# Optimization experiments

Hardware: AMD Instinct MI355X
Metric: run time of the kernel (lower is better)

Reference implementation:

```python
import jax, jax.numpy as jnp
import numpy as np

BN_EPS = 1e-5
GRID_W = 17  # conv output width hardcoded via lat_idx*17+lon_idx

def _conv(x, w, b, stride):
    y = jax.lax.conv_general_dilated(x, w, (stride, stride), [(1, 1), (1, 1)],
                                     dimension_numbers=("NCHW", "OIHW", "NCHW"))
    return y + b[None, :, None, None]

def _bn_eval(x, g, b):
    # running_mean=0, running_var=1 (fresh BatchNorm in eval mode)
    inv = jnp.float32(1.0 / np.sqrt(1.0 + BN_EPS))
    return x * (g[None, :, None, None] * inv) + b[None, :, None, None]

def setup_inputs() -> dict:
    key = jax.random.key(0)
    ks = iter(jax.random.split(key, 64))
    def rn(shape, s=0.05):
        return jax.random.normal(next(ks), shape, jnp.float32) * s
    B, S, K = 512, 128, 64
    NR = 100000
    inp = {}
    inp["roads"] = jax.random.randint(next(ks), (B, S), 0, NR)
    inp["ratios"] = jax.random.uniform(next(ks), (B, S), jnp.float32) * 0.9 + 0.1
    inp["T"] = jax.random.normal(next(ks), (1, 1, 138, 138), jnp.float32)
    inp["lon_idx"] = jax.random.randint(next(ks), (B, K), 0, 17)
    inp["lat_idx"] = jax.random.randint(next(ks), (B, K), 0, 17)
    inp["lengths"] = jax.random.uniform(next(ks), (NR,), jnp.float32) * 100.0 + 1.0
    inp["map_u"] = jnp.arange(NR, dtype=jnp.int32)
    inp["map_s1"] = jax.random.randint(next(ks), (NR,), 0, 14)
    inp["map_s2"] = jax.random.randint(next(ks), (NR,), 0, 7)
    inp["map_s3"] = jax.random.randint(next(ks), (NR,), 0, 2)
    inp["emb_u"] = rn((NR, 128))
    inp["emb_s1"] = rn((14, 16)); inp["emb_s2"] = rn((7, 8)); inp["emb_s3"] = rn((2, 4))
    inp["rho_w1"] = rn((156, 512)); inp["rho_b1"] = jnp.zeros((512,), jnp.float32)
    inp["rho_w21"] = rn((512, 128)); inp["rho_b21"] = jnp.zeros((128,), jnp.float32)
    inp["conv1_w"] = rn((32, 1, 5, 5)); inp["conv1_b"] = jnp.zeros((32,), jnp.float32)
    inp["bn1_g"] = jnp.ones((32,), jnp.float32); inp["bn1_b"] = jnp.zeros((32,), jnp.float32)
    inp["conv2_w"] = rn((64, 32, 4, 4)); inp["conv2_b"] = jnp.zeros((64,), jnp.float32)
    inp["bn2_g"] = jnp.ones((64,), jnp.float32); inp["bn2_b"] = jnp.zeros((64,), jnp.float32)
    inp["conv3_w"] = rn((128, 64, 4, 4)); inp["conv3_b"] = jnp.zeros((128,), jnp.float32)
    inp["bn3_g"] = jnp.ones((128,), jnp.float32); inp["bn3_b"] = jnp.zeros((128,), jnp.float32)
    inp["f2_w1"] = rn((128, 256)); inp["f2_b1"] = jnp.zeros((256,), jnp.float32)
    inp["f2_w2"] = rn((256, 128)); inp["f2_b2"] = jnp.zeros((128,), jnp.float32)
    inp["f_w1"] = rn((256, 512)); inp["f_b1"] = jnp.zeros((512,), jnp.float32)
    inp["f_w21"] = rn((512, 1)); inp["f_b21"] = jnp.zeros((1,), jnp.float32)
    inp["f_w22"] = rn((512, 1)); inp["f_b22"] = jnp.zeros((1,), jnp.float32)
    return inp

def reference(roads, ratios, T, lon_idx, lat_idx, lengths, map_u, map_s1, map_s2, map_s3,
              emb_u, emb_s1, emb_s2, emb_s3, rho_w1, rho_b1, rho_w21, rho_b21,
              conv1_w, conv1_b, bn1_g, bn1_b, conv2_w, conv2_b, bn2_g, bn2_b,
              conv3_w, conv3_b, bn3_g, bn3_b, f2_w1, f2_b1, f2_w2, f2_b2,
              f_w1, f_b1, f_w21, f_b21, f_w22, f_b22):
    # road lengths / weights
    road_lens = lengths[roads] * ratios               # (B,S)
    l = road_lens.sum(axis=1)                         # (B,)
    w = road_lens / l[:, None]                        # (B,S)
    # ProbRho (eval: dropout=id, reparameterize -> mu)
    u = emb_u[map_u[roads]]                           # (B,S,128)
    s1 = emb_s1[map_s1[roads]]; s2 = emb_s2[map_s2[roads]]; s3 = emb_s3[map_s3[roads]]
    x = jnp.concatenate([u, s1, s2, s3], axis=2)      # (B,S,156)
    h = jax.nn.relu(x @ rho_w1 + rho_b1)
    rho = h @ rho_w21 + rho_b21                       # (B,S,128)
    # ProbTraffic_spatial conv stack
    t = jax.nn.leaky_relu(_bn_eval(_conv(T, conv1_w, conv1_b, 2), bn1_g, bn1_b), 0.1)
    t = jax.nn.leaky_relu(_bn_eval(_conv(t, conv2_w, conv2_b, 2), bn2_g, bn2_b), 0.1)
    t = jax.nn.leaky_relu(_bn_eval(_conv(t, conv3_w, conv3_b, 2), bn3_g, bn3_b), 0.1)  # (1,128,17,17)
    c_flat = jnp.transpose(t[0], (1, 2, 0)).reshape(-1, t.shape[1])  # (289,128)
    # fused segment gather + mean over each trajectory's grid cells
    idx = lat_idx * GRID_W + lon_idx                  # (B,K)
    c_mean = c_flat[idx].mean(axis=1)                 # (B,128)
    h2 = jax.nn.selu(c_mean @ f2_w1 + f2_b1)
    c2 = h2 @ f2_w2 + f2_b2                           # (B,128)
    # ProbTravelTime
    xcat = jnp.concatenate([rho, jnp.broadcast_to(c2[:, None, :], rho.shape)], axis=2)  # (B,S,256)
    h3 = jax.nn.relu(xcat @ f_w1 + f_b1)              # (B,S,512)
    logm = (h3 @ f_w21 + f_b21)[..., 0]               # (B,S)
    logv = (h3 @ f_w22 + f_b22)[..., 0]
    logw = jnp.log(w)
    logm_agg = jax.nn.logsumexp(logm + logw, axis=1)
    logv_agg = jax.nn.logsumexp(logv + 2.0 * logw, axis=1)
    logl = jnp.log(l)
    logmu = logl - logm_agg
    loglam = logl - 3.0 * logm_agg - logv_agg
    return (logmu, loglam)
```

## Files before the change

kernel.cpp:

```cpp
#include <hip/hip_runtime.h>
#include <math.h>

#define BB 512
#define SS 128
#define NROWS (BB*SS)
#define TMG 128
#define NBLKG (NROWS/TMG)

__device__ __forceinline__ float leaky01(float x){ return x >= 0.f ? x : 0.1f*x; }

#define BN_INV 0.9999950000374997f
#define SELU_A 1.6732632423543772f
#define SELU_S 1.0507009873554805f

typedef __attribute__((ext_vector_type(8))) short short8;
typedef __attribute__((ext_vector_type(4))) float f32x4;

__device__ __forceinline__ unsigned short f2bf(float f) {
    unsigned int u = __float_as_uint(f);
    u += 0x7fff + ((u >> 16) & 1);
    return (unsigned short)(u >> 16);
}
__device__ __forceinline__ uint2 pack4bf(float a, float b, float c, float d) {
    uint2 r;
    r.x = (unsigned int)f2bf(a) | ((unsigned int)f2bf(b) << 16);
    r.y = (unsigned int)f2bf(c) | ((unsigned int)f2bf(d) << 16);
    return r;
}

__device__ __forceinline__ unsigned short* xsp(unsigned short* base, int row, int col) {
    unsigned off = (unsigned)(row*384 + col*2);
    off ^= (unsigned)((row & 7) << 4);
    return (unsigned short*)((char*)base + off);
}
__device__ __forceinline__ unsigned short* h1p(unsigned short* base, int row, int col) {
    unsigned off = (unsigned)(row*1024 + col*2);
    off ^= (unsigned)((row & 7) << 4);
    return (unsigned short*)((char*)base + off);
}
__device__ __forceinline__ unsigned short* xcp(unsigned short* base, int row, int col) {
    unsigned off = (unsigned)(row*512 + col*2);
    off ^= (unsigned)((row & 7) << 4);
    return (unsigned short*)((char*)base + off);
}

#define PREP_N (278528 + 32768 + 131072)
#define PREP_BLOCKS (PREP_N/256)
#define CONV1_BLOCKS 578

__global__ __launch_bounds__(256) void combo1_kernel(
    const float* __restrict__ w1, const float* __restrict__ w21, const float* __restrict__ fw1,
    unsigned short* __restrict__ sw1, unsigned short* __restrict__ sw21, unsigned short* __restrict__ sw3,
    const float* __restrict__ c2w_in, const float* __restrict__ c3w_in,
    float* __restrict__ w2t, float* __restrict__ w3t,
    const float* __restrict__ T, const float* __restrict__ cw,
    const float* __restrict__ cbias, const float* __restrict__ g,
    const float* __restrict__ bb, float* __restrict__ out)
{
    if (blockIdx.x < PREP_BLOCKS) {
        int t = blockIdx.x*256 + threadIdx.x;
        if (t < 81920) {
            int j = t & 7; int r = t >> 3; int lane = r & 63; r >>= 6;
            int ks = r % 5; int nt = r / 5;
            int n = nt*16 + (lane & 15);
            int k = ks*32 + (lane >> 4)*8 + j;
            float v = (k < 156) ? w1[k*512 + n] : 0.f;
            sw1[t] = f2bf(v);
        } else if (t < 147456) {
            int u = t - 81920;
            int j = u & 7; int r = u >> 3; int lane = r & 63; r >>= 6;
            int ks = r & 15; int nt = r >> 4;
            int d = nt*16 + (lane & 15);
            int k = ks*32 + (lane >> 4)*8 + j;
            sw21[u] = f2bf(w21[k*128 + d]);
        } else if (t < 278528) {
            int u = t - 147456;
            int j = u & 7; int r = u >> 3; int lane = r & 63; r >>= 6;
            int ks = r & 7; int nt = r >> 3;
            int n = nt*16 + (lane & 15);
            int k = ks*32 + (lane >> 4)*8 + j;
            sw3[u] = f2bf(fw1[k*512 + n]);
        } else if (t < 278528 + 32768) {
            int u = t - 278528;
            int oc = u >> 9; int r = u & 511;
            int kk = r >> 5; int ic = r & 31;
            w2t[u] = c2w_in[oc*512 + ic*16 + kk];
        } else {
            int u = t - (278528 + 32768);
            int oc = u >> 10; int r = u & 1023;
            int kk = r >> 6; int ic = r & 63;
            w3t[u] = c3w_in[oc*1024 + ic*16 + kk];
        }
    } else {
        int t = (blockIdx.x - PREP_BLOCKS)*256 + threadIdx.x;
        if (t >= 32*68*68) return;
        int oc  = t & 31;
        int pos = t >> 5;
        int oy = pos / 68, ox = pos % 68;
        float acc = cbias[oc];
        #pragma unroll
        for (int ky=0; ky<5; ++ky) {
            int iy = oy*2 - 1 + ky;
            if (iy < 0 || iy >= 138) continue;
            #pragma unroll
            for (int kx=0; kx<5; ++kx) {
                int ix = ox*2 - 1 + kx;
                if (ix < 0 || ix >= 138) continue;
                acc += cw[oc*25 + ky*5 + kx] * T[iy*138 + ix];
            }
        }
        acc = acc * (g[oc]*BN_INV) + bb[oc];
        out[pos*32 + oc] = leaky01(acc);
    }
}

__global__ __launch_bounds__(256) void conv2_kernel(
    const float* __restrict__ in,
    const float* __restrict__ w2t,
    const float* __restrict__ bias, const float* __restrict__ g,
    const float* __restrict__ bb, float* __restrict__ out)
{
    int gid = blockIdx.x*256 + threadIdx.x;
    if (gid >= 64*34*34*4) return;
    int icg = gid & 3;
    int o   = gid >> 2;
    int oc  = o & 63;
    int pos = o >> 6;
    int oy = pos / 34, ox = pos % 34;
    float acc = 0.f;
    #pragma unroll
    for (int ky=0; ky<4; ++ky) {
        int iy = oy*2 - 1 + ky;
        if (iy < 0 || iy >= 68) continue;
        #pragma unroll
        for (int kx=0; kx<4; ++kx) {
            int ix = ox*2 - 1 + kx;
            if (ix < 0 || ix >= 68) continue;
            const float* ip = &in[(iy*68+ix)*32 + icg*8];
            const float* wp = &w2t[oc*512 + (ky*4+kx)*32 + icg*8];
            float4 i0 = *(const float4*)ip, i1 = *(const float4*)(ip+4);
            float4 w0 = *(const float4*)wp, w1v = *(const float4*)(wp+4);
            acc += i0.x*w0.x + i0.y*w0.y + i0.z*w0.z + i0.w*w0.w
                 + i1.x*w1v.x + i1.y*w1v.y + i1.z*w1v.z + i1.w*w1v.w;
        }
    }
    acc += __shfl_xor(acc, 1, 64);
    acc += __shfl_xor(acc, 2, 64);
    if (icg == 0) {
        acc = (acc + bias[oc]) * (g[oc]*BN_INV) + bb[oc];
        out[pos*64 + oc] = leaky01(acc);
    }
}

__global__ __launch_bounds__(256) void conv3_kernel(
    const float* __restrict__ in,
    const float* __restrict__ w3t,
    const float* __restrict__ bias, const float* __restrict__ g,
    const float* __restrict__ bb, float* __restrict__ outT)
{
    int gid = blockIdx.x*256 + threadIdx.x;
    if (gid >= 128*289*8) return;
    int icg = gid & 7;
    int o   = gid >> 3;
    int oc  = o & 127;
    int pos = o >> 7;
    int oy = pos / 17, ox = pos % 17;
    float acc = 0.f;
    #pragma unroll
    for (int ky=0; ky<4; ++ky) {
        int iy = oy*2 - 1 + ky;
        if (iy < 0 || iy >= 34) continue;
        #pragma unroll
        for (int kx=0; kx<4; ++kx) {
            int ix = ox*2 - 1 + kx;
            if (ix < 0 || ix >= 34) continue;
            const float* ip = &in[(iy*34+ix)*64 + icg*8];
            const float* wp = &w3t[oc*1024 + (ky*4+kx)*64 + icg*8];
            float4 i0 = *(const float4*)ip, i1 = *(const float4*)(ip+4);
            float4 w0 = *(const float4*)wp, w1v = *(const float4*)(wp+4);
            acc += i0.x*w0.x + i0.y*w0.y + i0.z*w0.z + i0.w*w0.w
                 + i1.x*w1v.x + i1.y*w1v.y + i1.z*w1v.z + i1.w*w1v.w;
        }
    }
    acc += __shfl_xor(acc, 1, 64);
    acc += __shfl_xor(acc, 2, 64);
    acc += __shfl_xor(acc, 4, 64);
    if (icg == 0) {
        acc = (acc + bias[oc]) * (g[oc]*BN_INV) + bb[oc];
        outT[pos*128 + oc] = leaky01(acc);
    }
}

__global__ __launch_bounds__(256) void cmh2c2_kernel(
    const float* __restrict__ t3T, const int* __restrict__ lat, const int* __restrict__ lon,
    const float* __restrict__ w1, const float* __restrict__ b1,
    const float* __restrict__ w2, const float* __restrict__ b2,
    float* __restrict__ c2b)
{
    __shared__ int   ps[64];
    __shared__ float part[256];
    __shared__ float cms[128];
    __shared__ float h2s[256];
    const int b = blockIdx.x;
    const int tid = threadIdx.x;
    if (tid < 64) ps[tid] = lat[b*64+tid]*17 + lon[b*64+tid];
    __syncthreads();
    {
        int d = tid & 127, half = tid >> 7;
        float s = 0.f;
        #pragma unroll 8
        for (int k=0; k<32; ++k) s += t3T[ps[half*32+k]*128 + d];
        part[tid] = s;
    }
    __syncthreads();
    if (tid < 128) cms[tid] = (part[tid] + part[tid+128]) * (1.f/64.f);
    __syncthreads();
    {
        float acc = b1[tid];
        #pragma unroll 8
        for (int k=0; k<128; ++k) acc += cms[k] * w1[k*256 + tid];
        h2s[tid] = acc > 0.f ? SELU_S*acc : SELU_S*SELU_A*(expf(acc)-1.f);
    }
    __syncthreads();
    {
        int d = tid & 127, half = tid >> 7;
        float acc = 0.f;
        #pragma unroll 8
        for (int k=0; k<128; ++k) acc += h2s[half*128 + k] * w2[(half*128+k)*128 + d];
        part[tid] = acc;
    }
    __syncthreads();
    if (tid < 128) c2b[b*128 + tid] = part[tid] + part[tid+128] + b2[tid];
}

__global__ __launch_bounds__(1024, 4) void mega_kernel(
    const int* __restrict__ roads, const float* __restrict__ ratios,
    const float* __restrict__ lengths,
    const int* __restrict__ map_u, const int* __restrict__ map_s1,
    const int* __restrict__ map_s2, const int* __restrict__ map_s3,
    const float* __restrict__ emb_u, const float* __restrict__ emb_s1,
    const float* __restrict__ emb_s2, const float* __restrict__ emb_s3,
    const unsigned short* __restrict__ sw1, const float* __restrict__ b1,
    const unsigned short* __restrict__ sw21, const float* __restrict__ b21,
    const float* __restrict__ c2,
    const unsigned short* __restrict__ sw3, const float* __restrict__ fb1,
    const float* __restrict__ fw21, const float* __restrict__ fb21,
    const float* __restrict__ fw22, const float* __restrict__ fb22,
    float* __restrict__ out)
{
    __shared__ unsigned short buf[65536];
    float* pmv = (float*)buf;
    float* fin = (float*)buf + 4096;

    const int tid  = threadIdx.x;
    const int wid  = tid >> 6;
    const int lane = tid & 63;
    const int lo   = lane & 15;
    const int hi   = lane >> 4;
    const int b    = blockIdx.x;
    const int r0   = b * TMG;

    short8 afp[2];
    #pragma unroll
    for (int mt=0;mt<2;++mt)
        afp[mt] = *(const short8*)&sw1[((wid*2+mt)*5 + 0)*512 + lane*8];

    {
        int row = tid >> 3, seg = tid & 7;
        int road = roads[r0 + row];
        const float* src = emb_u + (long)map_u[road]*128 + seg*16;
        #pragma unroll
        for (int i=0;i<4;++i) {
            float4 v = *(const float4*)&src[i*4];
            *(uint2*)xsp(buf, row, seg*16 + i*4) = pack4bf(v.x, v.y, v.z, v.w);
        }
    }
    for (int idx = tid; idx < 128*32; idx += 1024) {
        int row = idx >> 5, k2 = idx & 31;
        int road = roads[r0 + row];
        float v;
        if      (k2 < 16) v = emb_s1[map_s1[road]*16 + k2];
        else if (k2 < 24) v = emb_s2[map_s2[road]*8  + (k2-16)];
        else if (k2 < 28) v = emb_s3[map_s3[road]*4  + (k2-24)];
        else              v = 0.f;
        *xsp(buf, row, 128 + k2) = f2bf(v);
    }
    __syncthreads();

    short8 a2p;
    f32x4 acc1[2][8];
    {
        #pragma unroll
        for (int mt=0;mt<2;++mt)
            #pragma unroll
            for (int rg=0;rg<8;++rg) acc1[mt][rg]=(f32x4)(0.f);
        #pragma unroll
        for (int ks=0; ks<5; ++ks) {
            const int kb = ks*32 + hi*8;
            short8 af[2];
            if (ks == 0) { af[0]=afp[0]; af[1]=afp[1]; }
            else {
                #pragma unroll
                for (int mt=0;mt<2;++mt)
                    af[mt] = *(const short8*)&sw1[((wid*2+mt)*5 + ks)*512 + lane*8];
            }
            #pragma unroll
            for (int rg=0;rg<8;++rg) {
                short8 bf = *(const short8*)xsp(buf, rg*16+lo, kb);
                acc1[0][rg] = __builtin_amdgcn_mfma_f32_16x16x32_bf16(af[0], bf, acc1[0][rg], 0,0,0);
                acc1[1][rg] = __builtin_amdgcn_mfma_f32_16x16x32_bf16(af[1], bf, acc1[1][rg], 0,0,0);
            }
        }
    }
    __syncthreads();

    {
        a2p = *(const short8*)&sw21[((wid>>1)*16 + 0)*512 + lane*8];
        const int n0 = wid * 32;
        #pragma unroll
        for (int mt=0;mt<2;++mt) {
            const int nb = n0 + mt*16 + hi*4;
            float4 bias = *(const float4*)&b1[nb];
            const float* bp = (const float*)&bias;
            #pragma unroll
            for (int rg=0;rg<8;++rg) {
                const float* a = (const float*)&acc1[mt][rg];
                float y0 = fmaxf(a[0]+bp[0], 0.f), y1 = fmaxf(a[1]+bp[1], 0.f);
                float y2 = fmaxf(a[2]+bp[2], 0.f), y3 = fmaxf(a[3]+bp[3], 0.f);
                *(uint2*)h1p(buf, rg*16+lo, nb) = pack4bf(y0,y1,y2,y3);
            }
        }
    }
    __syncthreads();

    short8 a3p[2];
    f32x4 acc2[4];
    const int nt2 = wid >> 1;
    const int rh  = wid & 1;
    {
        #pragma unroll
        for (int i=0;i<4;++i) acc2[i]=(f32x4)(0.f);
        #pragma unroll 4
        for (int ks=0; ks<16; ++ks) {
            const int kb = ks*32 + hi*8;
            short8 a = (ks == 0) ? a2p
                     : *(const short8*)&sw21[(nt2*16 + ks)*512 + lane*8];
            #pragma unroll
            for (int i=0;i<4;++i) {
                short8 bf = *(const short8*)h1p(buf, (rh*4+i)*16+lo, kb);
                acc2[i] = __builtin_amdgcn_mfma_f32_16x16x32_bf16(a, bf, acc2[i], 0,0,0);
            }
        }
    }
    __syncthreads();

    {
        #pragma unroll
        for (int mt=0;mt<2;++mt)
            a3p[mt] = *(const short8*)&sw3[((wid*2+mt)*8 + 0)*512 + lane*8];
        const int nb = nt2*16 + hi*4;
        float4 bias = *(const float4*)&b21[nb];
        const float* bp = (const float*)&bias;
        #pragma unroll
        for (int i=0;i<4;++i) {
            const float* a = (const float*)&acc2[i];
            *(uint2*)xcp(buf, (rh*4+i)*16+lo, nb) =
                pack4bf(a[0]+bp[0], a[1]+bp[1], a[2]+bp[2], a[3]+bp[3]);
        }
        int row = tid >> 3, seg = tid & 7;
        const float* src = c2 + b*128 + seg*16;
        #pragma unroll
        for (int i=0;i<4;++i) {
            float4 v = *(const float4*)&src[i*4];
            *(uint2*)xcp(buf, row, 128 + seg*16 + i*4) = pack4bf(v.x, v.y, v.z, v.w);
        }
    }
    __syncthreads();

    float sm[8], sv[8];
    {
        const int n0 = wid * 32;
        f32x4 acc[2][8];
        #pragma unroll
        for (int mt=0;mt<2;++mt)
            #pragma unroll
            for (int rg=0;rg<8;++rg) acc[mt][rg]=(f32x4)(0.f);
        #pragma unroll 2
        for (int ks=0; ks<8; ++ks) {
            const int kb = ks*32 + hi*8;
            short8 af[2];
            if (ks == 0) { af[0]=a3p[0]; af[1]=a3p[1]; }
            else {
                #pragma unroll
                for (int mt=0;mt<2;++mt)
                    af[mt] = *(const short8*)&sw3[((wid*2+mt)*8 + ks)*512 + lane*8];
            }
            #pragma unroll
            for (int rg=0;rg<8;++rg) {
                short8 bf = *(const short8*)xcp(buf, rg*16+lo, kb);
                acc[0][rg] = __builtin_amdgcn_mfma_f32_16x16x32_bf16(af[0], bf, acc[0][rg], 0,0,0);
                acc[1][rg] = __builtin_amdgcn_mfma_f32_16x16x32_bf16(af[1], bf, acc[1][rg], 0,0,0);
            }
        }
        #pragma unroll
        for (int rg=0;rg<8;++rg){ sm[rg]=0.f; sv[rg]=0.f; }
        #pragma unroll
        for (int mt=0;mt<2;++mt) {
            const int nb = n0 + mt*16 + hi*4;
            float4 bias = *(const float4*)&fb1[nb];
            float4 wm   = *(const float4*)&fw21[nb];
            float4 wv   = *(const float4*)&fw22[nb];
            const float *bp=(const float*)&bias, *wmp=(const float*)&wm, *wvp=(const float*)&wv;
            #pragma unroll
            for (int rg=0;rg<8;++rg) {
                const float* a = (const float*)&acc[mt][rg];
                #pragma unroll
                for (int j=0;j<4;++j) {
                    float y = fmaxf(a[j]+bp[j], 0.f);
                    sm[rg] += y*wmp[j];
                    sv[rg] += y*wvp[j];
                }
            }
        }
        #pragma unroll
        for (int rg=0;rg<8;++rg) {
            sm[rg] += __shfl_xor(sm[rg], 16, 64); sm[rg] += __shfl_xor(sm[rg], 32, 64);
            sv[rg] += __shfl_xor(sv[rg], 16, 64); sv[rg] += __shfl_xor(sv[rg], 32, 64);
        }
    }
    __syncthreads();
    if (hi == 0) {
        #pragma unroll
        for (int rg=0;rg<8;++rg) {
            pmv[wid*128 + rg*16 + lo]        = sm[rg];
            pmv[2048 + wid*128 + rg*16 + lo] = sv[rg];
        }
    }
    __syncthreads();

    float rl = 0.f, am = 0.f, av = 0.f;
    if (tid < 128) {
        float s_m = 0.f, s_v = 0.f;
        #pragma unroll
        for (int w=0; w<16; ++w) {
            s_m += pmv[w*128 + tid];
            s_v += pmv[2048 + w*128 + tid];
        }
        s_m += fb21[0]; s_v += fb22[0];
        int gi = r0 + tid;
        rl = lengths[roads[gi]] * ratios[gi];
        float ws = rl;
        #pragma unroll
        for (int off=32; off; off>>=1) ws += __shfl_xor(ws, off, 64);
        if (lane == 0) fin[wid] = ws;
        am = s_m; av = s_v;
    }
    __syncthreads();
    if (tid < 128) {
        float l = fin[0] + fin[1];
        float logl = logf(l);
        float lw = logf(rl) - logl;
        am += lw; av += 2.f*lw;
        fin[16] = logl;
        float mm = am, mv = av;
        #pragma unroll
        for (int off=32; off; off>>=1) { mm = fmaxf(mm, __shfl_xor(mm, off, 64)); mv = fmaxf(mv, __shfl_xor(mv, off, 64)); }
        if (lane == 0) { fin[2+wid] = mm; fin[4+wid] = mv; fin[8+wid] = logl; }
    }
    __syncthreads();
    if (tid < 128) {
        float mm = fmaxf(fin[2], fin[3]);
        float mv = fmaxf(fin[4], fin[5]);
        float se = expf(am - mm), sev = expf(av - mv);
        #pragma unroll
        for (int off=32; off; off>>=1) { se += __shfl_xor(se, off, 64); sev += __shfl_xor(sev, off, 64); }
        if (lane == 0) { fin[10+wid] = se; fin[12+wid] = sev; }
    }
    __syncthreads();
    if (tid == 0) {
        float mm = fmaxf(fin[2], fin[3]);
        float mv = fmaxf(fin[4], fin[5]);
        float lsem = logf(fin[10] + fin[11]) + mm;
        float lsev = logf(fin[12] + fin[13]) + mv;
        float logl = fin[8];
        out[b]       = logl - lsem;
        out[512 + b] = logl - 3.f*lsem - lsev;
    }
}

extern "C" void kernel_launch(void* const* d_in, const int* in_sizes, int n_in,
                              void* d_out, int out_size, void* d_ws, size_t ws_size,
                              hipStream_t stream) {
    const int*   roads   = (const int*)  d_in[0];
    const float* ratios  = (const float*)d_in[1];
    const float* T       = (const float*)d_in[2];
    const int*   lon_idx = (const int*)  d_in[3];
    const int*   lat_idx = (const int*)  d_in[4];
    const float* lengths = (const float*)d_in[5];
    const int*   map_u   = (const int*)  d_in[6];
    const int*   map_s1  = (const int*)  d_in[7];
    const int*   map_s2  = (const int*)  d_in[8];
    const int*   map_s3  = (const int*)  d_in[9];
    const float* emb_u   = (const float*)d_in[10];
    const float* emb_s1  = (const float*)d_in[11];
    const float* emb_s2  = (const float*)d_in[12];
    const float* emb_s3  = (const float*)d_in[13];
    const float* rho_w1  = (const float*)d_in[14];
    const float* rho_b1  = (const float*)d_in[15];
    const float* rho_w21 = (const float*)d_in[16];
    const float* rho_b21 = (const float*)d_in[17];
    const float* conv1_w = (const float*)d_in[18];
    const float* conv1_b = (const float*)d_in[19];
    const float* bn1_g   = (const float*)d_in[20];
    const float* bn1_b   = (const float*)d_in[21];
    const float* conv2_w = (const float*)d_in[22];
    const float* conv2_b = (const float*)d_in[23];
    const float* bn2_g   = (const float*)d_in[24];
    const float* bn2_b   = (const float*)d_in[25];
    const float* conv3_w = (const float*)d_in[26];
    const float* conv3_b = (const float*)d_in[27];
    const float* bn3_g   = (const float*)d_in[28];
    const float* bn3_b   = (const float*)d_in[29];
    const float* f2_w1   = (const float*)d_in[30];
    const float* f2_b1   = (const float*)d_in[31];
    const float* f2_w2   = (const float*)d_in[32];
    const float* f2_b2   = (const float*)d_in[33];
    const float* f_w1    = (const float*)d_in[34];
    const float* f_b1    = (const float*)d_in[35];
    const float* f_w21   = (const float*)d_in[36];
    const float* f_b21   = (const float*)d_in[37];
    const float* f_w22   = (const float*)d_in[38];
    const float* f_b22   = (const float*)d_in[39];

    float* ws    = (float*)d_ws;
    float* t1    = ws;
    float* t2    = t1 + 147968;
    float* t3T   = t2 + 73984;
    float* c2b   = t3T + 36992;
    float* w2t   = c2b + 65536;
    float* w3t   = w2t + 32768;
    unsigned short* sw1  = (unsigned short*)(w3t + 131072);
    unsigned short* sw21 = sw1 + 81920;
    unsigned short* sw3  = sw21 + 65536;

    combo1_kernel<<<PREP_BLOCKS + CONV1_BLOCKS, 256, 0, stream>>>(
        rho_w1, rho_w21, f_w1, sw1, sw21, sw3,
        conv2_w, conv3_w, w2t, w3t,
        T, conv1_w, conv1_b, bn1_g, bn1_b, t1);
    conv2_kernel<<<(64*34*34*4 + 255)/256, 256, 0, stream>>>(t1, w2t, conv2_b, bn2_g, bn2_b, t2);
    conv3_kernel<<<(128*289*8 + 255)/256, 256, 0, stream>>>(t2, w3t, conv3_b, bn3_g, bn3_b, t3T);
    cmh2c2_kernel<<<512, 256, 0, stream>>>(t3T, lat_idx, lon_idx, f2_w1, f2_b1, f2_w2, f2_b2, c2b);
    mega_kernel<<<NBLKG, 1024, 0, stream>>>(roads, ratios, lengths,
                                            map_u, map_s1, map_s2, map_s3,
                                            emb_u, emb_s1, emb_s2, emb_s3,
                                            sw1, rho_b1, sw21, rho_b21,
                                            c2b, sw3, f_b1, f_w21, f_b21, f_w22, f_b22,
                                            (float*)d_out);
}
```

Measured before the change: 117.2 us.

## Fold broadcast c2 half of f_w1 into per-batch bias; prefetch MFMA A-fragments

The c2 half of the concatenated input to f_w1 is the same for all rows of a batch. Its product with the lower 128 rows of f_w1 is now computed once per batch in cmh2c2_kernel and stored as a per-batch 512-wide bias, which halves the K dimension of the third GEMM in mega_kernel. The three MFMA loops are also fully unrolled, with A-fragment loads issued two or four steps ahead and B-fragment LDS reads batched. bf16 packing now uses the HIP intrinsic, and the xcp stride shrinks to match the halved K. The extra fp32 per-batch GEMV costs a little more in cmh2c2, and the deeper prefetch raises register pressure.

```diff
diff --git a/kernel.cpp b/kernel.cpp
--- a/kernel.cpp
+++ b/kernel.cpp
@@ -1,4 +1,5 @@
 #include <hip/hip_runtime.h>
+#include <hip/hip_bf16.h>
 #include <math.h>
 
 #define BB 512
@@ -21,11 +22,14 @@
     u += 0x7fff + ((u >> 16) & 1);
     return (unsigned short)(u >> 16);
 }
+__device__ __forceinline__ unsigned int pk2(float a, float b) {
+    __hip_bfloat162 h = __float22bfloat162_rn(make_float2(a, b));
+    unsigned int u;
+    __builtin_memcpy(&u, &h, 4);
+    return u;
+}
 __device__ __forceinline__ uint2 pack4bf(float a, float b, float c, float d) {
-    uint2 r;
-    r.x = (unsigned int)f2bf(a) | ((unsigned int)f2bf(b) << 16);
-    r.y = (unsigned int)f2bf(c) | ((unsigned int)f2bf(d) << 16);
-    return r;
+    uint2 r; r.x = pk2(a, b); r.y = pk2(c, d); return r;
 }
 
 __device__ __forceinline__ unsigned short* xsp(unsigned short* base, int row, int col) {
@@ -39,7 +43,7 @@
     return (unsigned short*)((char*)base + off);
 }
 __device__ __forceinline__ unsigned short* xcp(unsigned short* base, int row, int col) {
-    unsigned off = (unsigned)(row*512 + col*2);
+    unsigned off = (unsigned)(row*256 + col*2);
     off ^= (unsigned)((row & 7) << 4);
     return (unsigned short*)((char*)base + off);
 }
@@ -195,12 +199,14 @@
     const float* __restrict__ t3T, const int* __restrict__ lat, const int* __restrict__ lon,
     const float* __restrict__ w1, const float* __restrict__ b1,
     const float* __restrict__ w2, const float* __restrict__ b2,
-    float* __restrict__ c2b)
+    const float* __restrict__ fw1, const float* __restrict__ fb1,
+    float* __restrict__ cvb)
 {
     __shared__ int   ps[64];
     __shared__ float part[256];
     __shared__ float cms[128];
     __shared__ float h2s[256];
+    __shared__ float c2s[128];
     const int b = blockIdx.x;
     const int tid = threadIdx.x;
     if (tid < 64) ps[tid] = lat[b*64+tid]*17 + lon[b*64+tid];
@@ -230,7 +236,19 @@
         part[tid] = acc;
     }
     __syncthreads();
-    if (tid < 128) c2b[b*128 + tid] = part[tid] + part[tid+128] + b2[tid];
+    if (tid < 128) c2s[tid] = part[tid] + part[tid+128] + b2[tid];
+    __syncthreads();
+    {
+        float a0 = fb1[tid], a1 = fb1[tid + 256];
+        #pragma unroll 8
+        for (int k=0; k<128; ++k) {
+            float c = c2s[k];
+            a0 += c * fw1[(128+k)*512 + tid];
+            a1 += c * fw1[(128+k)*512 + 256 + tid];
+        }
+        cvb[b*512 + tid]       = a0;
+        cvb[b*512 + 256 + tid] = a1;
+    }
 }
 
 __global__ __launch_bounds__(1024, 4) void mega_kernel(
@@ -242,8 +260,7 @@
     const float* __restrict__ emb_s2, const float* __restrict__ emb_s3,
     const unsigned short* __restrict__ sw1, const float* __restrict__ b1,
     const unsigned short* __restrict__ sw21, const float* __restrict__ b21,
-    const float* __restrict__ c2,
-    const unsigned short* __restrict__ sw3, const float* __restrict__ fb1,
+    const unsigned short* __restrict__ sw3, const float* __restrict__ cvb,
     const float* __restrict__ fw21, const float* __restrict__ fb21,
     const float* __restrict__ fw22, const float* __restrict__ fb22,
     float* __restrict__ out)
@@ -259,11 +276,13 @@
     const int hi   = lane >> 4;
     const int b    = blockIdx.x;
     const int r0   = b * TMG;
-
-    short8 afp[2];
-    #pragma unroll
-    for (int mt=0;mt<2;++mt)
-        afp[mt] = *(const short8*)&sw1[((wid*2+mt)*5 + 0)*512 + lane*8];
+    const int nt2  = wid >> 1;
+    const int rh   = wid & 1;
+
+    short8 afp00 = *(const short8*)&sw1[((wid*2+0)*5 + 0)*512 + lane*8];
+    short8 afp10 = *(const short8*)&sw1[((wid*2+1)*5 + 0)*512 + lane*8];
+    short8 afp01 = *(const short8*)&sw1[((wid*2+0)*5 + 1)*512 + lane*8];
+    short8 afp11 = *(const short8*)&sw1[((wid*2+1)*5 + 1)*512 + lane*8];
 
     {
         int row = tid >> 3, seg = tid & 7;
@@ -287,35 +306,47 @@
     }
     __syncthreads();
 
-    short8 a2p;
     f32x4 acc1[2][8];
     {
         #pragma unroll
         for (int mt=0;mt<2;++mt)
             #pragma unroll
             for (int rg=0;rg<8;++rg) acc1[mt][rg]=(f32x4)(0.f);
+        short8 a0c = afp00, a1c = afp10, a0n = afp01, a1n = afp11;
         #pragma unroll
         for (int ks=0; ks<5; ++ks) {
+            short8 a0f = a0c, a1f = a1c;
+            if (ks < 3) {
+                a0f = *(const short8*)&sw1[((wid*2+0)*5 + ks+2)*512 + lane*8];
+                a1f = *(const short8*)&sw1[((wid*2+1)*5 + ks+2)*512 + lane*8];
+            }
             const int kb = ks*32 + hi*8;
-            short8 af[2];
-            if (ks == 0) { af[0]=afp[0]; af[1]=afp[1]; }
-            else {
-                #pragma unroll
-                for (int mt=0;mt<2;++mt)
-                    af[mt] = *(const short8*)&sw1[((wid*2+mt)*5 + ks)*512 + lane*8];
-            }
-            #pragma unroll
-            for (int rg=0;rg<8;++rg) {
-                short8 bf = *(const short8*)xsp(buf, rg*16+lo, kb);
-                acc1[0][rg] = __builtin_amdgcn_mfma_f32_16x16x32_bf16(af[0], bf, acc1[0][rg], 0,0,0);
-                acc1[1][rg] = __builtin_amdgcn_mfma_f32_16x16x32_bf16(af[1], bf, acc1[1][rg], 0,0,0);
-            }
-        }
-    }
-    __syncthreads();
-
-    {
-        a2p = *(const short8*)&sw21[((wid>>1)*16 + 0)*512 + lane*8];
+            short8 bf[4];
+            #pragma unroll
+            for (int rg=0;rg<4;++rg) bf[rg] = *(const short8*)xsp(buf, rg*16+lo, kb);
+            #pragma unroll
+            for (int rg=0;rg<4;++rg) {
+                acc1[0][rg] = __builtin_amdgcn_mfma_f32_16x16x32_bf16(a0c, bf[rg], acc1[0][rg], 0,0,0);
+                acc1[1][rg] = __builtin_amdgcn_mfma_f32_16x16x32_bf16(a1c, bf[rg], acc1[1][rg], 0,0,0);
+            }
+            #pragma unroll
+            for (int rg=0;rg<4;++rg) bf[rg] = *(const short8*)xsp(buf, (4+rg)*16+lo, kb);
+            #pragma unroll
+            for (int rg=0;rg<4;++rg) {
+                acc1[0][4+rg] = __builtin_amdgcn_mfma_f32_16x16x32_bf16(a0c, bf[rg], acc1[0][4+rg], 0,0,0);
+                acc1[1][4+rg] = __builtin_amdgcn_mfma_f32_16x16x32_bf16(a1c, bf[rg], acc1[1][4+rg], 0,0,0);
+            }
+            a0c = a0n; a1c = a1n; a0n = a0f; a1n = a1f;
+        }
+    }
+    __syncthreads();
+
+    short8 a2q0, a2q1, a2q2, a2q3;
+    {
+        a2q0 = *(const short8*)&sw21[(nt2*16 + 0)*512 + lane*8];
+        a2q1 = *(const short8*)&sw21[(nt2*16 + 1)*512 + lane*8];
+        a2q2 = *(const short8*)&sw21[(nt2*16 + 2)*512 + lane*8];
+        a2q3 = *(const short8*)&sw21[(nt2*16 + 3)*512 + lane*8];
         const int n0 = wid * 32;
         #pragma unroll
         for (int mt=0;mt<2;++mt) {
@@ -333,31 +364,33 @@
     }
     __syncthreads();
 
-    short8 a3p[2];
     f32x4 acc2[4];
-    const int nt2 = wid >> 1;
-    const int rh  = wid & 1;
     {
         #pragma unroll
         for (int i=0;i<4;++i) acc2[i]=(f32x4)(0.f);
-        #pragma unroll 4
+        #pragma unroll
         for (int ks=0; ks<16; ++ks) {
+            short8 a_use = a2q0;
+            a2q0 = a2q1; a2q1 = a2q2; a2q2 = a2q3;
+            if (ks < 12)
+                a2q3 = *(const short8*)&sw21[(nt2*16 + ks+4)*512 + lane*8];
             const int kb = ks*32 + hi*8;
-            short8 a = (ks == 0) ? a2p
-                     : *(const short8*)&sw21[(nt2*16 + ks)*512 + lane*8];
-            #pragma unroll
-            for (int i=0;i<4;++i) {
-                short8 bf = *(const short8*)h1p(buf, (rh*4+i)*16+lo, kb);
-                acc2[i] = __builtin_amdgcn_mfma_f32_16x16x32_bf16(a, bf, acc2[i], 0,0,0);
-            }
-        }
-    }
-    __syncthreads();
-
-    {
-        #pragma unroll
-        for (int mt=0;mt<2;++mt)
-            a3p[mt] = *(const short8*)&sw3[((wid*2+mt)*8 + 0)*512 + lane*8];
+            short8 bf[4];
+            #pragma unroll
+            for (int i=0;i<4;++i) bf[i] = *(const short8*)h1p(buf, (rh*4+i)*16+lo, kb);
+            #pragma unroll
+            for (int i=0;i<4;++i)
+                acc2[i] = __builtin_amdgcn_mfma_f32_16x16x32_bf16(a_use, bf[i], acc2[i], 0,0,0);
+        }
+    }
+    __syncthreads();
+
+    short8 a3c0, a3c1, a3n0, a3n1;
+    {
+        a3c0 = *(const short8*)&sw3[((wid*2+0)*8 + 0)*512 + lane*8];
+        a3c1 = *(const short8*)&sw3[((wid*2+1)*8 + 0)*512 + lane*8];
+        a3n0 = *(const short8*)&sw3[((wid*2+0)*8 + 1)*512 + lane*8];
+        a3n1 = *(const short8*)&sw3[((wid*2+1)*8 + 1)*512 + lane*8];
         const int nb = nt2*16 + hi*4;
         float4 bias = *(const float4*)&b21[nb];
         const float* bp = (const float*)&bias;
@@ -367,13 +400,6 @@
             *(uint2*)xcp(buf, (rh*4+i)*16+lo, nb) =
                 pack4bf(a[0]+bp[0], a[1]+bp[1], a[2]+bp[2], a[3]+bp[3]);
         }
-        int row = tid >> 3, seg = tid & 7;
-        const float* src = c2 + b*128 + seg*16;
-        #pragma unroll
-        for (int i=0;i<4;++i) {
-            float4 v = *(const float4*)&src[i*4];
-            *(uint2*)xcp(buf, row, 128 + seg*16 + i*4) = pack4bf(v.x, v.y, v.z, v.w);
-        }
     }
     __syncthreads();
 
@@ -385,29 +411,37 @@
         for (int mt=0;mt<2;++mt)
             #pragma unroll
             for (int rg=0;rg<8;++rg) acc[mt][rg]=(f32x4)(0.f);
-        #pragma unroll 2
-        for (int ks=0; ks<8; ++ks) {
+        #pragma unroll
+        for (int ks=0; ks<4; ++ks) {
+            short8 c0f = a3c0, c1f = a3c1;
+            if (ks < 2) {
+                c0f = *(const short8*)&sw3[((wid*2+0)*8 + ks+2)*512 + lane*8];
+                c1f = *(const short8*)&sw3[((wid*2+1)*8 + ks+2)*512 + lane*8];
+            }
             const int kb = ks*32 + hi*8;
-            short8 af[2];
-            if (ks == 0) { af[0]=a3p[0]; af[1]=a3p[1]; }
-            else {
-                #pragma unroll
-                for (int mt=0;mt<2;++mt)
-                    af[mt] = *(const short8*)&sw3[((wid*2+mt)*8 + ks)*512 + lane*8];
-            }
-            #pragma unroll
-            for (int rg=0;rg<8;++rg) {
-                short8 bf = *(const short8*)xcp(buf, rg*16+lo, kb);
-                acc[0][rg] = __builtin_amdgcn_mfma_f32_16x16x32_bf16(af[0], bf, acc[0][rg], 0,0,0);
-                acc[1][rg] = __builtin_amdgcn_mfma_f32_16x16x32_bf16(af[1], bf, acc[1][rg], 0,0,0);
-            }
+            short8 bf[4];
+            #pragma unroll
+            for (int rg=0;rg<4;++rg) bf[rg] = *(const short8*)xcp(buf, rg*16+lo, kb);
+            #pragma unroll
+            for (int rg=0;rg<4;++rg) {
+                acc[0][rg] = __builtin_amdgcn_mfma_f32_16x16x32_bf16(a3c0, bf[rg], acc[0][rg], 0,0,0);
+                acc[1][rg] = __builtin_amdgcn_mfma_f32_16x16x32_bf16(a3c1, bf[rg], acc[1][rg], 0,0,0);
+            }
+            #pragma unroll
+            for (int rg=0;rg<4;++rg) bf[rg] = *(const short8*)xcp(buf, (4+rg)*16+lo, kb);
+            #pragma unroll
+            for (int rg=0;rg<4;++rg) {
+                acc[0][4+rg] = __builtin_amdgcn_mfma_f32_16x16x32_bf16(a3c0, bf[rg], acc[0][4+rg], 0,0,0);
+                acc[1][4+rg] = __builtin_amdgcn_mfma_f32_16x16x32_bf16(a3c1, bf[rg], acc[1][4+rg], 0,0,0);
+            }
+            a3c0 = a3n0; a3c1 = a3n1; a3n0 = c0f; a3n1 = c1f;
         }
         #pragma unroll
         for (int rg=0;rg<8;++rg){ sm[rg]=0.f; sv[rg]=0.f; }
         #pragma unroll
         for (int mt=0;mt<2;++mt) {
             const int nb = n0 + mt*16 + hi*4;
-            float4 bias = *(const float4*)&fb1[nb];
+            float4 bias = *(const float4*)&cvb[b*512 + nb];
             float4 wm   = *(const float4*)&fw21[nb];
             float4 wv   = *(const float4*)&fw22[nb];
             const float *bp=(const float*)&bias, *wmp=(const float*)&wm, *wvp=(const float*)&wv;
@@ -461,7 +495,6 @@
         float logl = logf(l);
         float lw = logf(rl) - logl;
         am += lw; av += 2.f*lw;
-        fin[16] = logl;
         float mm = am, mv = av;
         #pragma unroll
         for (int off=32; off; off>>=1) { mm = fmaxf(mm, __shfl_xor(mm, off, 64)); mv = fmaxf(mv, __shfl_xor(mv, off, 64)); }
@@ -536,8 +569,8 @@
     float* t1    = ws;
     float* t2    = t1 + 147968;
     float* t3T   = t2 + 73984;
-    float* c2b   = t3T + 36992;
-    float* w2t   = c2b + 65536;
+    float* cvb   = t3T + 36992;
+    float* w2t   = cvb + 262144;
     float* w3t   = w2t + 32768;
     unsigned short* sw1  = (unsigned short*)(w3t + 131072);
     unsigned short* sw21 = sw1 + 81920;
@@ -549,11 +582,12 @@
         T, conv1_w, conv1_b, bn1_g, bn1_b, t1);
     conv2_kernel<<<(64*34*34*4 + 255)/256, 256, 0, stream>>>(t1, w2t, conv2_b, bn2_g, bn2_b, t2);
     conv3_kernel<<<(128*289*8 + 255)/256, 256, 0, stream>>>(t2, w3t, conv3_b, bn3_g, bn3_b, t3T);
-    cmh2c2_kernel<<<512, 256, 0, stream>>>(t3T, lat_idx, lon_idx, f2_w1, f2_b1, f2_w2, f2_b2, c2b);
+    cmh2c2_kernel<<<512, 256, 0, stream>>>(t3T, lat_idx, lon_idx, f2_w1, f2_b1, f2_w2, f2_b2,
+                                           f_w1, f_b1, cvb);
     mega_kernel<<<NBLKG, 1024, 0, stream>>>(roads, ratios, lengths,
                                             map_u, map_s1, map_s2, map_s3,
                                             emb_u, emb_s1, emb_s2, emb_s3,
                                             sw1, rho_b1, sw21, rho_b21,
-                                            c2b, sw3, f_b1, f_w21, f_b21, f_w22, f_b22,
+                                            sw3, cvb, f_w21, f_b21, f_w22, f_b22,
                                             (float*)d_out);
 }
```

New measurement: 117.1 us, median of 2. No clear change (-0.0%).
